# Performance work log

Hardware: AMD Instinct MI355X
Metric: run time of the kernel (lower is better)

The kernel has to match this reference:

```python
import jax, jax.numpy as jnp
import numpy as np

HIDDEN = 2048
NUM_HEADS = 16
HEAD_DIM = HIDDEN // NUM_HEADS
INIT_RANGE = 0.02


def setup_inputs() -> dict:
    key = jax.random.key(0)
    ks = jax.random.split(key, 5)
    B, S = 2, 2048
    hidden_states = jax.random.normal(ks[0], (B, S, HIDDEN), dtype=jnp.float32)
    # Linear weights stored torch-style [out, in]; biases zero-init per _init_weights
    def w(k):
        return INIT_RANGE * jax.random.normal(k, (HIDDEN, HIDDEN), dtype=jnp.float32)
    return {
        "hidden_states": hidden_states,
        "wq": w(ks[1]), "bq": jnp.zeros((HIDDEN,), jnp.float32),
        "wk": w(ks[2]), "bk": jnp.zeros((HIDDEN,), jnp.float32),
        "wv": w(ks[3]), "bv": jnp.zeros((HIDDEN,), jnp.float32),
        "wo": w(ks[4]), "bo": jnp.zeros((HIDDEN,), jnp.float32),
    }


def _split_heads(x):
    # [B,S,H] -> [B,nh,S,hd]
    B, S, _ = x.shape
    return x.reshape(B, S, NUM_HEADS, HEAD_DIM).transpose(0, 2, 1, 3)


def reference(hidden_states, wq, bq, wk, bk, wv, bv, wo, bo):
    B, S, H = hidden_states.shape
    scale = 1.0 / np.sqrt(HEAD_DIM).astype(np.float32)

    q = _split_heads(hidden_states @ wq.T + bq)  # [B,nh,S,hd]
    k = _split_heads(hidden_states @ wk.T + bk)
    v = _split_heads(hidden_states @ wv.T + bv)

    attn = jnp.einsum('bhqd,bhkd->bhqk', q, k) * scale  # [B,nh,S,S]
    # causal mask: -inf above diagonal, 0 on/below
    causal = jnp.where(
        jnp.tril(jnp.ones((S, S), dtype=bool)),
        jnp.float32(0.0), jnp.float32(-jnp.inf))
    attn = attn + causal
    probs = jax.nn.softmax(attn, axis=-1)
    out = jnp.einsum('bhqk,bhkd->bhqd', probs, v)  # [B,nh,S,hd]
    out = out.transpose(0, 2, 1, 3).reshape(B, S, H)  # merge heads
    return out @ wo.T + bo
```

## Files before the change

### kernel.cpp

```cpp
#include <hip/hip_runtime.h>
#include <stdint.h>

typedef unsigned short u16;
typedef __attribute__((ext_vector_type(8))) short short8;
typedef __attribute__((ext_vector_type(4))) short short4v;
typedef __attribute__((ext_vector_type(4))) float float4v;

union V8u { short8 v; short4v h[2]; u16 u[8]; unsigned w[4]; };

__device__ __forceinline__ u16 f2bf(float f) {
  unsigned u = __float_as_uint(f);
  u = u + 0x7FFFu + ((u >> 16) & 1u);
  return (u16)(u >> 16);
}
__device__ __forceinline__ float4v fzero() {
  float4v z = {0.f, 0.f, 0.f, 0.f};
  return z;
}
__device__ __forceinline__ void gl_lds16(const u16* g, u16* l) {
  __builtin_amdgcn_global_load_lds(
      (const __attribute__((address_space(1))) void*)g,
      (__attribute__((address_space(3))) void*)l, 16, 0, 0);
}

#define MFMA16(a, b, c) __builtin_amdgcn_mfma_f32_16x16x32_bf16((a), (b), (c), 0, 0, 0)

__global__ void conv_f32_bf16(const float* __restrict__ in, u16* __restrict__ out, long n) {
  const long i = ((long)blockIdx.x * 256 + threadIdx.x) * 8;
  if (i >= n) return;
  float4 a = *(const float4*)&in[i];
  float4 b = *(const float4*)&in[i + 4];
  V8u o;
  o.u[0] = f2bf(a.x); o.u[1] = f2bf(a.y); o.u[2] = f2bf(a.z); o.u[3] = f2bf(a.w);
  o.u[4] = f2bf(b.x); o.u[5] = f2bf(b.y); o.u[6] = f2bf(b.z); o.u[7] = f2bf(b.w);
  *(short8*)&out[i] = o.v;
}

__global__ void conv3_f32_bf16(const float* __restrict__ s0, const float* __restrict__ s1,
                               const float* __restrict__ s2, u16* __restrict__ dst, long n) {
  const float* s = (blockIdx.y == 0) ? s0 : (blockIdx.y == 1 ? s1 : s2);
  u16* d = dst + (long)blockIdx.y * n;
  const long i = ((long)blockIdx.x * 256 + threadIdx.x) * 8;
  if (i >= n) return;
  float4 a = *(const float4*)&s[i];
  float4 b = *(const float4*)&s[i + 4];
  V8u o;
  o.u[0] = f2bf(a.x); o.u[1] = f2bf(a.y); o.u[2] = f2bf(a.z); o.u[3] = f2bf(a.w);
  o.u[4] = f2bf(b.x); o.u[5] = f2bf(b.y); o.u[6] = f2bf(b.z); o.u[7] = f2bf(b.w);
  *(short8*)&d[i] = o.v;
}

template <bool OUTF32>
__global__ __launch_bounds__(256, 2) void gemm_bt_bias(
    const u16* __restrict__ X,
    const u16* __restrict__ W0, const float* __restrict__ B0, void* __restrict__ O0,
    const u16* __restrict__ W1, const float* __restrict__ B1, void* __restrict__ O1,
    const u16* __restrict__ W2, const float* __restrict__ B2, void* __restrict__ O2,
    int M, int N, int K)
{
  const u16* W = W0; const float* Bb = B0; void* Ov = O0;
  if (blockIdx.z == 1) { W = W1; Bb = B1; Ov = O1; }
  else if (blockIdx.z == 2) { W = W2; Bb = B2; Ov = O2; }

  __shared__ u16 As[128 * 32];
  __shared__ u16 Bs[128 * 32];

  const int t = threadIdx.x;
  const int lane = t & 63, wave = t >> 6;
  const int quad = lane >> 4, l16 = lane & 15;
  const int wm = wave >> 1, wn = wave & 1;
  const long m0 = (long)blockIdx.y * 128;
  const long n0 = (long)blockIdx.x * 128;

  const int srow = t >> 2;
  const int scol = (t & 3) * 8;

  float4v acc[4][4];
  #pragma unroll
  for (int i = 0; i < 4; ++i)
    #pragma unroll
    for (int j = 0; j < 4; ++j) acc[i][j] = fzero();

  for (int k0 = 0; k0 < K; k0 += 32) {
    gl_lds16(&X[(m0 + srow) * K + k0 + scol],      &As[t * 8]);
    gl_lds16(&X[(m0 + srow + 64) * K + k0 + scol], &As[t * 8 + 64 * 32]);
    gl_lds16(&W[(n0 + srow) * K + k0 + scol],      &Bs[t * 8]);
    gl_lds16(&W[(n0 + srow + 64) * K + k0 + scol], &Bs[t * 8 + 64 * 32]);
    __syncthreads();

    short8 a[4], b[4];
    #pragma unroll
    for (int mi = 0; mi < 4; ++mi)
      a[mi] = *(const short8*)&As[(wm * 64 + mi * 16 + l16) * 32 + quad * 8];
    #pragma unroll
    for (int ni = 0; ni < 4; ++ni)
      b[ni] = *(const short8*)&Bs[(wn * 64 + ni * 16 + l16) * 32 + quad * 8];
    #pragma unroll
    for (int mi = 0; mi < 4; ++mi)
      #pragma unroll
      for (int ni = 0; ni < 4; ++ni)
        acc[mi][ni] = MFMA16(a[mi], b[ni], acc[mi][ni]);
    __syncthreads();
  }

  #pragma unroll
  for (int ni = 0; ni < 4; ++ni) {
    const long cg = n0 + wn * 64 + ni * 16 + l16;
    const float bv = Bb[cg];
    #pragma unroll
    for (int mi = 0; mi < 4; ++mi) {
      const long rg0 = m0 + wm * 64 + mi * 16 + quad * 4;
      #pragma unroll
      for (int r = 0; r < 4; ++r) {
        const float v = acc[mi][ni][r] + bv;
        if (OUTF32) ((float*)Ov)[(rg0 + r) * N + cg] = v;
        else        ((u16*)Ov)[(rg0 + r) * N + cg] = f2bf(v);
      }
    }
  }
}

#define S_LEN 2048
#define HID   2048
#define HD    128

__global__ __launch_bounds__(256, 4) void attn_fwd(
    const u16* __restrict__ Q, const u16* __restrict__ K,
    const u16* __restrict__ V, u16* __restrict__ Ctx)
{
  __shared__ u16 Ks[2][32 * 136];
  __shared__ unsigned Vt[2][128 * 17];
  __shared__ u16 Ps[4 * 16 * 32];

  const int t = threadIdx.x;
  const int lane = t & 63, wave = t >> 6;
  const int quad = lane >> 4, l16 = lane & 15;
  const int qb = (int)(gridDim.x - 1 - blockIdx.x) * 64;
  const int b = blockIdx.y >> 4, h = blockIdx.y & 15;

  const long base = (long)b * S_LEN * HID + (long)h * HD;
  const u16* Qp = Q + base;
  const u16* Kp = K + base;
  const u16* Vp = V + base;

  const int sr2 = t >> 4;
  const int sc8 = (t & 15) * 8;

  short8 qf[4];
  {
    const long qr = qb + wave * 16 + l16;
    #pragma unroll
    for (int kk = 0; kk < 4; ++kk)
      qf[kk] = *(const short8*)&Qp[qr * HID + kk * 32 + quad * 8];
  }

  short8 onesv;
  {
    V8u ou;
    #pragma unroll
    for (int j = 0; j < 8; ++j) ou.u[j] = 0x3F80;
    onesv = ou.v;
  }

  float4v o[9];
  #pragma unroll
  for (int i = 0; i < 9; ++i) o[i] = fzero();
  const float SC = 0.08838834764831845f * 1.4426950408889634f;

  short8 kr0, kr1, vv0, vv1;
  {
    const long g = (long)(2 * sr2) * HID + sc8;
    kr0 = *(const short8*)&Kp[g];
    kr1 = *(const short8*)&Kp[g + HID];
    vv0 = *(const short8*)&Vp[g];
    vv1 = *(const short8*)&Vp[g + HID];
  }
  {
    *(short8*)&Ks[0][(2 * sr2) * 136 + sc8]     = kr0;
    *(short8*)&Ks[0][(2 * sr2 + 1) * 136 + sc8] = kr1;
    V8u a, c; a.v = vv0; c.v = vv1;
    #pragma unroll
    for (int j = 0; j < 8; ++j)
      Vt[0][(sc8 + j) * 17 + sr2] = (unsigned)a.u[j] | ((unsigned)c.u[j] << 16);
  }
  __syncthreads();

  const int T = (qb + 64) >> 5;
  for (int ti = 0; ti < T; ++ti) {
    const int kv0 = ti << 5;
    const int p = ti & 1;

    const bool more = (ti + 1 < T);
    if (more) {
      const long g = (long)(kv0 + 32 + 2 * sr2) * HID + sc8;
      kr0 = *(const short8*)&Kp[g];
      kr1 = *(const short8*)&Kp[g + HID];
      vv0 = *(const short8*)&Vp[g];
      vv1 = *(const short8*)&Vp[g + HID];
    }

    if (kv0 <= qb + wave * 16) {
      float4v s[2] = {fzero(), fzero()};
      #pragma unroll
      for (int ni = 0; ni < 2; ++ni)
        #pragma unroll
        for (int kk = 0; kk < 4; ++kk) {
          short8 kf = *(const short8*)&Ks[p][(ni * 16 + l16) * 136 + kk * 32 + quad * 8];
          s[ni] = MFMA16(qf[kk], kf, s[ni]);
        }

      const int qrow0 = qb + wave * 16 + quad * 4;
      float p0[4], p1[4];
      #pragma unroll
      for (int r = 0; r < 4; ++r) {
        float s0 = fminf(s[0][r] * SC, 80.f);
        float s1 = fminf(s[1][r] * SC, 80.f);
        if (kv0 + l16 > qrow0 + r)      s0 = -1e30f;
        if (kv0 + 16 + l16 > qrow0 + r) s1 = -1e30f;
        p0[r] = __builtin_amdgcn_exp2f(s0);
        p1[r] = __builtin_amdgcn_exp2f(s1);
      }

      const int pb = wave * 512;
      #pragma unroll
      for (int r = 0; r < 4; ++r) {
        Ps[pb + (quad * 4 + r) * 32 + l16]      = f2bf(p0[r]);
        Ps[pb + (quad * 4 + r) * 32 + 16 + l16] = f2bf(p1[r]);
      }
      __threadfence_block();
      short8 pf = *(const short8*)&Ps[pb + l16 * 32 + quad * 8];

      #pragma unroll
      for (int dt = 0; dt < 8; ++dt) {
        const unsigned* vp = &Vt[p][(dt * 16 + l16) * 17 + quad * 4];
        V8u vf;
        vf.w[0] = vp[0]; vf.w[1] = vp[1]; vf.w[2] = vp[2]; vf.w[3] = vp[3];
        o[dt] = MFMA16(pf, vf.v, o[dt]);
      }
      o[8] = MFMA16(pf, onesv, o[8]);
    }

    if (more) {
      *(short8*)&Ks[1 - p][(2 * sr2) * 136 + sc8]     = kr0;
      *(short8*)&Ks[1 - p][(2 * sr2 + 1) * 136 + sc8] = kr1;
      V8u a, c; a.v = vv0; c.v = vv1;
      #pragma unroll
      for (int j = 0; j < 8; ++j)
        Vt[1 - p][(sc8 + j) * 17 + sr2] = (unsigned)a.u[j] | ((unsigned)c.u[j] << 16);
    }
    __syncthreads();
  }

  u16* Cp = Ctx + base;
  #pragma unroll
  for (int r = 0; r < 4; ++r) {
    const float inv = 1.0f / o[8][r];
    const long qr = qb + wave * 16 + quad * 4 + r;
    #pragma unroll
    for (int dt = 0; dt < 8; ++dt)
      Cp[qr * HID + dt * 16 + l16] = f2bf(o[dt][r] * inv);
  }
}

extern "C" void kernel_launch(void* const* d_in, const int* in_sizes, int n_in,
                              void* d_out, int out_size, void* d_ws, size_t ws_size,
                              hipStream_t stream) {
  const float* X  = (const float*)d_in[0];
  const float* wq = (const float*)d_in[1];
  const float* bq = (const float*)d_in[2];
  const float* wk = (const float*)d_in[3];
  const float* bk = (const float*)d_in[4];
  const float* wv = (const float*)d_in[5];
  const float* bv = (const float*)d_in[6];
  const float* wo = (const float*)d_in[7];
  const float* bo = (const float*)d_in[8];
  float* out = (float*)d_out;

  const long HSZ = 4096L * 2048;
  const long WSZ = 2048L * 2048;
  u16* Qw = (u16*)d_ws;
  u16* Kw = Qw + HSZ;
  u16* Vw = Kw + HSZ;
  u16* Xb = Vw + HSZ;
  u16* Wb = Xb + HSZ;
  u16* W0 = Wb, *W1 = Wb + WSZ, *W2 = Wb + 2 * WSZ;

  dim3 blk(256);
  conv_f32_bf16<<<(int)(HSZ / 2048), blk, 0, stream>>>(X, Xb, HSZ);
  conv3_f32_bf16<<<dim3((int)(WSZ / 2048), 3), blk, 0, stream>>>(wq, wk, wv, Wb, WSZ);

  gemm_bt_bias<false><<<dim3(16, 32, 3), blk, 0, stream>>>(
      Xb, W0, bq, Qw, W1, bk, Kw, W2, bv, Vw, 4096, 2048, 2048);

  attn_fwd<<<dim3(32, 32), blk, 0, stream>>>(Qw, Kw, Vw, Qw);

  conv_f32_bf16<<<(int)(WSZ / 2048), blk, 0, stream>>>(wo, W0, WSZ);
  gemm_bt_bias<true><<<dim3(16, 32, 1), blk, 0, stream>>>(
      Qw, W0, bo, out, W0, bo, out, W0, bo, out, 4096, 2048, 2048);
}
```

Measured before the change: 474.8 us.

## Double per-wave query rows in attention and merge input conversion launches

The attention kernel now gives each wave 32 query rows (two 16-row groups) and each block 128 rows. Every K/V tile loaded into shared memory therefore feeds twice as many MFMAs, and the grid shrinks to 16x32 blocks. Occupancy drops to two blocks per CU and register use roughly doubles for the accumulators. Separately, the X and Wq/Wk/Wv fp32-to-bf16 conversions are merged into one five-segment launch, which relies on Xb and Wb being contiguous in the workspace.

```diff
diff --git a/kernel.cpp b/kernel.cpp
--- a/kernel.cpp
+++ b/kernel.cpp
@@ -24,6 +24,25 @@
 }
 
 #define MFMA16(a, b, c) __builtin_amdgcn_mfma_f32_16x16x32_bf16((a), (b), (c), 0, 0, 0)
+
+__global__ void conv5_f32_bf16(const float* __restrict__ X,
+                               const float* __restrict__ w0,
+                               const float* __restrict__ w1,
+                               const float* __restrict__ w2,
+                               u16* __restrict__ dst, long seg) {
+  const int y = blockIdx.y;
+  const float* s = (y < 2) ? (X + (long)y * seg)
+                           : (y == 2 ? w0 : (y == 3 ? w1 : w2));
+  u16* d = dst + (long)y * seg;
+  const long i = ((long)blockIdx.x * 256 + threadIdx.x) * 8;
+  if (i >= seg) return;
+  float4 a = *(const float4*)&s[i];
+  float4 b = *(const float4*)&s[i + 4];
+  V8u o;
+  o.u[0] = f2bf(a.x); o.u[1] = f2bf(a.y); o.u[2] = f2bf(a.z); o.u[3] = f2bf(a.w);
+  o.u[4] = f2bf(b.x); o.u[5] = f2bf(b.y); o.u[6] = f2bf(b.z); o.u[7] = f2bf(b.w);
+  *(short8*)&d[i] = o.v;
+}
 
 __global__ void conv_f32_bf16(const float* __restrict__ in, u16* __restrict__ out, long n) {
   const long i = ((long)blockIdx.x * 256 + threadIdx.x) * 8;
@@ -34,20 +53,6 @@
   o.u[0] = f2bf(a.x); o.u[1] = f2bf(a.y); o.u[2] = f2bf(a.z); o.u[3] = f2bf(a.w);
   o.u[4] = f2bf(b.x); o.u[5] = f2bf(b.y); o.u[6] = f2bf(b.z); o.u[7] = f2bf(b.w);
   *(short8*)&out[i] = o.v;
-}
-
-__global__ void conv3_f32_bf16(const float* __restrict__ s0, const float* __restrict__ s1,
-                               const float* __restrict__ s2, u16* __restrict__ dst, long n) {
-  const float* s = (blockIdx.y == 0) ? s0 : (blockIdx.y == 1 ? s1 : s2);
-  u16* d = dst + (long)blockIdx.y * n;
-  const long i = ((long)blockIdx.x * 256 + threadIdx.x) * 8;
-  if (i >= n) return;
-  float4 a = *(const float4*)&s[i];
-  float4 b = *(const float4*)&s[i + 4];
-  V8u o;
-  o.u[0] = f2bf(a.x); o.u[1] = f2bf(a.y); o.u[2] = f2bf(a.z); o.u[3] = f2bf(a.w);
-  o.u[4] = f2bf(b.x); o.u[5] = f2bf(b.y); o.u[6] = f2bf(b.z); o.u[7] = f2bf(b.w);
-  *(short8*)&d[i] = o.v;
 }
 
 template <bool OUTF32>
@@ -124,18 +129,18 @@
 #define HID   2048
 #define HD    128
 
-__global__ __launch_bounds__(256, 4) void attn_fwd(
+__global__ __launch_bounds__(256, 2) void attn_fwd(
     const u16* __restrict__ Q, const u16* __restrict__ K,
     const u16* __restrict__ V, u16* __restrict__ Ctx)
 {
   __shared__ u16 Ks[2][32 * 136];
   __shared__ unsigned Vt[2][128 * 17];
-  __shared__ u16 Ps[4 * 16 * 32];
+  __shared__ u16 Ps[4 * 2 * 512];
 
   const int t = threadIdx.x;
   const int lane = t & 63, wave = t >> 6;
   const int quad = lane >> 4, l16 = lane & 15;
-  const int qb = (int)(gridDim.x - 1 - blockIdx.x) * 64;
+  const int qb = (int)(gridDim.x - 1 - blockIdx.x) * 128;
   const int b = blockIdx.y >> 4, h = blockIdx.y & 15;
 
   const long base = (long)b * S_LEN * HID + (long)h * HD;
@@ -145,13 +150,15 @@
 
   const int sr2 = t >> 4;
   const int sc8 = (t & 15) * 8;
-
-  short8 qf[4];
-  {
-    const long qr = qb + wave * 16 + l16;
+  const int wqb = qb + wave * 32;
+
+  short8 qf[2][4];
+  #pragma unroll
+  for (int g = 0; g < 2; ++g) {
+    const long qr = wqb + g * 16 + l16;
     #pragma unroll
     for (int kk = 0; kk < 4; ++kk)
-      qf[kk] = *(const short8*)&Qp[qr * HID + kk * 32 + quad * 8];
+      qf[g][kk] = *(const short8*)&Qp[qr * HID + kk * 32 + quad * 8];
   }
 
   short8 onesv;
@@ -162,9 +169,11 @@
     onesv = ou.v;
   }
 
-  float4v o[9];
-  #pragma unroll
-  for (int i = 0; i < 9; ++i) o[i] = fzero();
+  float4v o[2][9];
+  #pragma unroll
+  for (int g = 0; g < 2; ++g)
+    #pragma unroll
+    for (int i = 0; i < 9; ++i) o[g][i] = fzero();
   const float SC = 0.08838834764831845f * 1.4426950408889634f;
 
   short8 kr0, kr1, vv0, vv1;
@@ -185,7 +194,7 @@
   }
   __syncthreads();
 
-  const int T = (qb + 64) >> 5;
+  const int T = (qb + 128) >> 5;
   for (int ti = 0; ti < T; ++ti) {
     const int kv0 = ti << 5;
     const int p = ti & 1;
@@ -199,45 +208,47 @@
       vv1 = *(const short8*)&Vp[g + HID];
     }
 
-    if (kv0 <= qb + wave * 16) {
-      float4v s[2] = {fzero(), fzero()};
+    if (kv0 <= wqb) {
+      float4v s[2][2];
+      #pragma unroll
+      for (int g = 0; g < 2; ++g) { s[g][0] = fzero(); s[g][1] = fzero(); }
       #pragma unroll
       for (int ni = 0; ni < 2; ++ni)
         #pragma unroll
         for (int kk = 0; kk < 4; ++kk) {
           short8 kf = *(const short8*)&Ks[p][(ni * 16 + l16) * 136 + kk * 32 + quad * 8];
-          s[ni] = MFMA16(qf[kk], kf, s[ni]);
+          s[0][ni] = MFMA16(qf[0][kk], kf, s[0][ni]);
+          s[1][ni] = MFMA16(qf[1][kk], kf, s[1][ni]);
         }
 
-      const int qrow0 = qb + wave * 16 + quad * 4;
-      float p0[4], p1[4];
-      #pragma unroll
-      for (int r = 0; r < 4; ++r) {
-        float s0 = fminf(s[0][r] * SC, 80.f);
-        float s1 = fminf(s[1][r] * SC, 80.f);
-        if (kv0 + l16 > qrow0 + r)      s0 = -1e30f;
-        if (kv0 + 16 + l16 > qrow0 + r) s1 = -1e30f;
-        p0[r] = __builtin_amdgcn_exp2f(s0);
-        p1[r] = __builtin_amdgcn_exp2f(s1);
-      }
-
-      const int pb = wave * 512;
-      #pragma unroll
-      for (int r = 0; r < 4; ++r) {
-        Ps[pb + (quad * 4 + r) * 32 + l16]      = f2bf(p0[r]);
-        Ps[pb + (quad * 4 + r) * 32 + 16 + l16] = f2bf(p1[r]);
+      const int pb = wave * 1024;
+      #pragma unroll
+      for (int g = 0; g < 2; ++g) {
+        const int qrow0 = wqb + g * 16 + quad * 4;
+        #pragma unroll
+        for (int r = 0; r < 4; ++r) {
+          float s0 = fminf(s[g][0][r] * SC, 80.f);
+          float s1 = fminf(s[g][1][r] * SC, 80.f);
+          if (kv0 + l16 > qrow0 + r)      s0 = -1e30f;
+          if (kv0 + 16 + l16 > qrow0 + r) s1 = -1e30f;
+          Ps[pb + g * 512 + (quad * 4 + r) * 32 + l16]      = f2bf(__builtin_amdgcn_exp2f(s0));
+          Ps[pb + g * 512 + (quad * 4 + r) * 32 + 16 + l16] = f2bf(__builtin_amdgcn_exp2f(s1));
+        }
       }
       __threadfence_block();
-      short8 pf = *(const short8*)&Ps[pb + l16 * 32 + quad * 8];
+      short8 pf0 = *(const short8*)&Ps[pb + l16 * 32 + quad * 8];
+      short8 pf1 = *(const short8*)&Ps[pb + 512 + l16 * 32 + quad * 8];
 
       #pragma unroll
       for (int dt = 0; dt < 8; ++dt) {
         const unsigned* vp = &Vt[p][(dt * 16 + l16) * 17 + quad * 4];
         V8u vf;
         vf.w[0] = vp[0]; vf.w[1] = vp[1]; vf.w[2] = vp[2]; vf.w[3] = vp[3];
-        o[dt] = MFMA16(pf, vf.v, o[dt]);
+        o[0][dt] = MFMA16(pf0, vf.v, o[0][dt]);
+        o[1][dt] = MFMA16(pf1, vf.v, o[1][dt]);
       }
-      o[8] = MFMA16(pf, onesv, o[8]);
+      o[0][8] = MFMA16(pf0, onesv, o[0][8]);
+      o[1][8] = MFMA16(pf1, onesv, o[1][8]);
     }
 
     if (more) {
@@ -253,13 +264,15 @@
 
   u16* Cp = Ctx + base;
   #pragma unroll
-  for (int r = 0; r < 4; ++r) {
-    const float inv = 1.0f / o[8][r];
-    const long qr = qb + wave * 16 + quad * 4 + r;
-    #pragma unroll
-    for (int dt = 0; dt < 8; ++dt)
-      Cp[qr * HID + dt * 16 + l16] = f2bf(o[dt][r] * inv);
-  }
+  for (int g = 0; g < 2; ++g)
+    #pragma unroll
+    for (int r = 0; r < 4; ++r) {
+      const float inv = 1.0f / o[g][8][r];
+      const long qr = wqb + g * 16 + quad * 4 + r;
+      #pragma unroll
+      for (int dt = 0; dt < 8; ++dt)
+        Cp[qr * HID + dt * 16 + l16] = f2bf(o[g][dt][r] * inv);
+    }
 }
 
 extern "C" void kernel_launch(void* const* d_in, const int* in_sizes, int n_in,
@@ -286,13 +299,12 @@
   u16* W0 = Wb, *W1 = Wb + WSZ, *W2 = Wb + 2 * WSZ;
 
   dim3 blk(256);
-  conv_f32_bf16<<<(int)(HSZ / 2048), blk, 0, stream>>>(X, Xb, HSZ);
-  conv3_f32_bf16<<<dim3((int)(WSZ / 2048), 3), blk, 0, stream>>>(wq, wk, wv, Wb, WSZ);
+  conv5_f32_bf16<<<dim3((int)(WSZ / 2048), 5), blk, 0, stream>>>(X, wq, wk, wv, Xb, WSZ);
 
   gemm_bt_bias<false><<<dim3(16, 32, 3), blk, 0, stream>>>(
       Xb, W0, bq, Qw, W1, bk, Kw, W2, bv, Vw, 4096, 2048, 2048);
 
-  attn_fwd<<<dim3(32, 32), blk, 0, stream>>>(Qw, Kw, Vw, Qw);
+  attn_fwd<<<dim3(16, 32), blk, 0, stream>>>(Qw, Kw, Vw, Qw);
 
   conv_f32_bf16<<<(int)(WSZ / 2048), blk, 0, stream>>>(wo, W0, WSZ);
   gemm_bt_bias<true><<<dim3(16, 32, 1), blk, 0, stream>>>(
```

Result: faster. 436.7 us (-8.0%).
